# Kernel optimization log

Hardware: AMD Instinct MI355X
Metric: run time of the kernel (lower is better)

Reference implementation:

```python
import jax, jax.numpy as jnp
import numpy as np

N_NODES = 100000
N_EDGES = 3200000
NFEAT, NHID, NCLASS = 512, 256, 40


def setup_inputs() -> dict:
    key = jax.random.key(0)
    ks = jax.random.split(key, 8)
    x = jax.random.normal(ks[0], (N_NODES, NFEAT), dtype=jnp.float32)
    edge_src = jax.random.randint(ks[1], (N_EDGES,), 0, N_NODES, dtype=jnp.int32)
    edge_dst = jax.random.randint(ks[2], (N_EDGES,), 0, N_NODES, dtype=jnp.int32)
    # normalized adjacency values (e.g. D^-1/2 A D^-1/2 entries)
    edge_weight = jax.random.uniform(ks[3], (N_EDGES,), dtype=jnp.float32)
    W1 = jax.random.normal(ks[4], (NFEAT, NHID), dtype=jnp.float32) * (1.0 / np.sqrt(NFEAT))
    b1 = jnp.zeros((NHID,), dtype=jnp.float32)
    W2 = jax.random.normal(ks[5], (NHID, NCLASS), dtype=jnp.float32) * (1.0 / np.sqrt(NHID))
    b2 = jnp.zeros((NCLASS,), dtype=jnp.float32)
    return {"x": x, "edge_src": edge_src, "edge_dst": edge_dst,
            "edge_weight": edge_weight, "W1": W1, "b1": b1, "W2": W2, "b2": b2}


def _gcn_conv(x, edge_src, edge_dst, edge_weight, W, b):
    # GCNConv: support = x @ W ; out = spmm(adj, support) + b
    support = x @ W                                   # [N, D_out]
    msgs = edge_weight[:, None] * support[edge_src]   # [E, D_out]
    agg = jax.ops.segment_sum(msgs, edge_dst, num_segments=x.shape[0])
    return agg + b


def reference(x, edge_src, edge_dst, edge_weight, W1, b1, W2, b2):
    h = jax.nn.relu(_gcn_conv(x, edge_src, edge_dst, edge_weight, W1, b1))
    # F.dropout with training=False is identity (eval/reference mode)
    h = _gcn_conv(h, edge_src, edge_dst, edge_weight, W2, b2)
    return jax.nn.log_softmax(h, axis=1)
```

## Files before the change

kernel.cpp:

```cpp
#include <hip/hip_runtime.h>
#include <hip/hip_bf16.h>
#include <math.h>


#define NFEAT 512
#define NHID  256
#define NCLASS 40
#define BKT_SHIFT 9
#define BKT_NODES 512
#define MAX_BKT 256
#define BIN_EPB 4096

typedef __attribute__((ext_vector_type(4))) float f32x4;
typedef __attribute__((ext_vector_type(8))) short s16x8;

__device__ __forceinline__ ushort f2bf(float f) {
  unsigned u = __float_as_uint(f);
  u = (u + 0x7fffu + ((u >> 16) & 1u)) >> 16;
  return (ushort)u;
}
__device__ __forceinline__ float bflo(unsigned u) {
  return __uint_as_float(u << 16);
}
__device__ __forceinline__ float bfhi(unsigned u) {
  return __uint_as_float(u & 0xffff0000u);
}

__global__ __launch_bounds__(256) void w1t_kernel(const float* __restrict__ W1,
                                                  ushort* __restrict__ Bt) {
  int idx = blockIdx.x * 256 + threadIdx.x;
  int k = idx >> 8, n = idx & 255;
  Bt[n * NFEAT + k] = f2bf(W1[idx]);
}

#define LDK 40
__global__ __launch_bounds__(256) void gemm1_mfma(
    const float* __restrict__ A, const ushort* __restrict__ Bt,
    ushort* __restrict__ C, int M) {
  __shared__ ushort As[128 * LDK];
  __shared__ ushort Bs[128 * LDK];
  int tid = threadIdx.x;
  int wave = tid >> 6, lane = tid & 63;
  int bm = blockIdx.y * 128;
  int bn = blockIdx.x * 128;
  int wm = (wave & 1) * 64, wn = (wave >> 1) * 64;
  int lm = lane & 15;
  int lk = (lane >> 4) * 8;

  int arow = tid >> 1;
  int ahalf = (tid & 1) * 16;
  int brow = tid >> 2;
  int bq = (tid & 3) * 8;

  f32x4 acc[4][4] = {};

  const bool arv = (bm + arow) < M;
  const float* aptr = A + (size_t)(bm + arow) * NFEAT + ahalf;
  ushort* asp = &As[arow * LDK + ahalf];

  for (int k0 = 0; k0 < NFEAT; k0 += 32) {
#pragma unroll
    for (int q = 0; q < 4; ++q) {
      float4 v = arv ? *(const float4*)(aptr + k0 + q * 4)
                     : make_float4(0.f, 0.f, 0.f, 0.f);
      ushort4 b;
      b.x = f2bf(v.x); b.y = f2bf(v.y); b.z = f2bf(v.z); b.w = f2bf(v.w);
      *(ushort4*)(asp + q * 4) = b;
    }
#pragma unroll
    for (int p = 0; p < 2; ++p) {
      int n = p * 64 + brow;
      *(uint4*)&Bs[n * LDK + bq] =
          *(const uint4*)&Bt[(size_t)(bn + n) * NFEAT + k0 + bq];
    }
    __syncthreads();
    s16x8 afr[4], bfr[4];
#pragma unroll
    for (int i = 0; i < 4; ++i)
      afr[i] = *(const s16x8*)&As[(wm + i * 16 + lm) * LDK + lk];
#pragma unroll
    for (int j = 0; j < 4; ++j)
      bfr[j] = *(const s16x8*)&Bs[(wn + j * 16 + lm) * LDK + lk];
#pragma unroll
    for (int i = 0; i < 4; ++i)
#pragma unroll
      for (int j = 0; j < 4; ++j)
        acc[i][j] = __builtin_amdgcn_mfma_f32_16x16x32_bf16(afr[i], bfr[j],
                                                            acc[i][j], 0, 0, 0);
    __syncthreads();
  }
  int ocol = bn + wn + lm;
  int orow0 = bm + wm + (lane >> 4) * 4;
#pragma unroll
  for (int i = 0; i < 4; ++i) {
#pragma unroll
    for (int r = 0; r < 4; ++r) {
      int row = orow0 + i * 16 + r;
      if (row < M) {
#pragma unroll
        for (int j = 0; j < 4; ++j)
          C[(size_t)row * NHID + ocol + j * 16] = f2bf(acc[i][j][r]);
      }
    }
  }
}

__global__ __launch_bounds__(256) void hist_kernel(const int* __restrict__ dst,
                                                   int* __restrict__ deg, int E) {
  int e = blockIdx.x * 256 + threadIdx.x;
  if (e < E) atomicAdd(&deg[dst[e]], 1);
}

__global__ __launch_bounds__(256) void scan1_kernel(const int* __restrict__ deg,
                                                    int* __restrict__ part,
                                                    int* __restrict__ bsums, int M) {
  __shared__ int tmp[256];
  int t = threadIdx.x;
  int i = blockIdx.x * 256 + t;
  int v = (i < M) ? deg[i] : 0;
  tmp[t] = v;
  __syncthreads();
  for (int off = 1; off < 256; off <<= 1) {
    int add = (t >= off) ? tmp[t - off] : 0;
    __syncthreads();
    tmp[t] += add;
    __syncthreads();
  }
  if (i < M) part[i] = tmp[t];
  if (t == 255) bsums[blockIdx.x] = tmp[255];
}

__global__ __launch_bounds__(512) void scan2_kernel(int* __restrict__ bsums, int nb) {
  __shared__ int tmp[512];
  int t = threadIdx.x;
  int v = (t < nb) ? bsums[t] : 0;
  tmp[t] = v;
  __syncthreads();
  for (int off = 1; off < 512; off <<= 1) {
    int add = (t >= off) ? tmp[t - off] : 0;
    __syncthreads();
    tmp[t] += add;
    __syncthreads();
  }
  if (t < nb) bsums[t] = tmp[t];
}

__global__ __launch_bounds__(256) void scan3_kernel(
    const int* __restrict__ part, const int* __restrict__ bsums,
    const int* __restrict__ deg, int* __restrict__ rowptr, int M) {
  int i = blockIdx.x * 256 + threadIdx.x;
  if (i >= M) return;
  int incl = part[i] + (blockIdx.x > 0 ? bsums[blockIdx.x - 1] : 0);
  rowptr[i] = incl - deg[i];
}

__global__ __launch_bounds__(256) void initcur_kernel(
    const int* __restrict__ rowptr, int* __restrict__ gcursor, int nbkt) {
  int b = threadIdx.x;
  if (b < nbkt) gcursor[b] = rowptr[b * BKT_NODES];
}

__global__ __launch_bounds__(256) void binA_kernel(
    const int* __restrict__ esrc, const int* __restrict__ edst,
    const float* __restrict__ ew, int* __restrict__ gcursor,
    int2* __restrict__ tmp_sw, ushort* __restrict__ tmp_d, int E) {
  __shared__ int hist[MAX_BKT];
  int t = threadIdx.x;
  for (int i = t; i < MAX_BKT; i += 256) hist[i] = 0;
  __syncthreads();
  int e0 = blockIdx.x * BIN_EPB;
#pragma unroll
  for (int k = 0; k < BIN_EPB / 256; ++k) {
    int e = e0 + k * 256 + t;
    if (e < E) atomicAdd(&hist[edst[e] >> BKT_SHIFT], 1);
  }
  __syncthreads();
  for (int i = t; i < MAX_BKT; i += 256) {
    int c = hist[i];
    hist[i] = c ? atomicAdd(&gcursor[i], c) : 0;
  }
  __syncthreads();
#pragma unroll
  for (int k = 0; k < BIN_EPB / 256; ++k) {
    int e = e0 + k * 256 + t;
    if (e < E) {
      int d = edst[e];
      int b = d >> BKT_SHIFT;
      int pos = atomicAdd(&hist[b], 1);
      tmp_sw[pos] = make_int2(esrc[e], __float_as_int(ew[e]));
      tmp_d[pos] = (ushort)(d & (BKT_NODES - 1));
    }
  }
}

__global__ __launch_bounds__(512) void binB_kernel(
    const int2* __restrict__ tmp_sw, const ushort* __restrict__ tmp_d,
    const int* __restrict__ rowptr, int2* __restrict__ ep, int M, int E) {
  __shared__ int cur[BKT_NODES];
  int b = blockIdx.x;
  int nbase = b * BKT_NODES;
  for (int i = threadIdx.x; i < BKT_NODES; i += 512) {
    int node = nbase + i;
    cur[i] = (node < M) ? rowptr[node] : 0;
  }
  __syncthreads();
  int start = rowptr[nbase];
  int nend = nbase + BKT_NODES;
  int end = (nend < M) ? rowptr[nend] : E;
  for (int i = start + threadIdx.x; i < end; i += 512) {
    int2 sw = tmp_sw[i];
    int dl = tmp_d[i];
    int pos = atomicAdd(&cur[dl], 1);
    ep[pos] = sw;
  }
}

__global__ __launch_bounds__(256) void spmm1_csr_kernel(
    const ushort* __restrict__ S, const int* __restrict__ rowptr,
    const int* __restrict__ deg, const int2* __restrict__ ep,
    const float* __restrict__ b1, ushort* __restrict__ h, int M) {
  int wid = (blockIdx.x * 256 + threadIdx.x) >> 6;
  int lane = threadIdx.x & 63;
  if (wid >= M) return;
  int beg = rowptr[wid];
  int n = deg[wid];
  const ushort* Sl = S + (size_t)lane * 4;
  float acc0 = 0.f, acc1 = 0.f, acc2 = 0.f, acc3 = 0.f;
  for (int j0 = 0; j0 < n; j0 += 64) {
    int cnt = min(64, n - j0);
    int msrc = 0;
    float mw = 0.f;
    if (lane < cnt) {
      int2 e = ep[beg + j0 + lane];
      msrc = e.x;
      mw = __int_as_float(e.y);
    }
    for (int j = 0; j < cnt; ++j) {
      int s = __shfl(msrc, j);
      float wt = __shfl(mw, j);
      uint2 u = *(const uint2*)(Sl + ((size_t)s << 8));
      acc0 += wt * bflo(u.x);
      acc1 += wt * bfhi(u.x);
      acc2 += wt * bflo(u.y);
      acc3 += wt * bfhi(u.y);
    }
  }
  float4 b = *(const float4*)(b1 + lane * 4);
  ushort4 o;
  o.x = f2bf(fmaxf(acc0 + b.x, 0.f));
  o.y = f2bf(fmaxf(acc1 + b.y, 0.f));
  o.z = f2bf(fmaxf(acc2 + b.z, 0.f));
  o.w = f2bf(fmaxf(acc3 + b.w, 0.f));
  *(ushort4*)(h + ((size_t)wid << 8) + lane * 4) = o;
}

__global__ __launch_bounds__(256) void gemm2_kernel(
    const ushort* __restrict__ H, const float* __restrict__ W2,
    ushort* __restrict__ S2, int M) {
  __shared__ float W2s[NHID * NCLASS];
  for (int i = threadIdx.x; i < NHID * NCLASS; i += 256) W2s[i] = W2[i];
  __syncthreads();
  int row = blockIdx.x * 256 + threadIdx.x;
  if (row >= M) return;
  const float4* W2v = (const float4*)W2s;
  float4 acc[10];
#pragma unroll
  for (int j = 0; j < 10; ++j) acc[j] = make_float4(0.f, 0.f, 0.f, 0.f);
  const uint4* hp = (const uint4*)(H + (size_t)row * NHID);
  for (int kb = 0; kb < 32; ++kb) {
    uint4 u = hp[kb];
    float a[8] = {bflo(u.x), bfhi(u.x), bflo(u.y), bfhi(u.y),
                  bflo(u.z), bfhi(u.z), bflo(u.w), bfhi(u.w)};
#pragma unroll
    for (int kk = 0; kk < 8; ++kk) {
#pragma unroll
      for (int j = 0; j < 10; ++j) {
        float4 wv = W2v[(kb * 8 + kk) * 10 + j];
        acc[j].x += a[kk] * wv.x;
        acc[j].y += a[kk] * wv.y;
        acc[j].z += a[kk] * wv.z;
        acc[j].w += a[kk] * wv.w;
      }
    }
  }
  uint2* outp = (uint2*)(S2 + (size_t)row * NCLASS);
#pragma unroll
  for (int j = 0; j < 10; j += 2) {
    uint2 o0, o1;
    o0.x = (unsigned)f2bf(acc[j].x) | ((unsigned)f2bf(acc[j].y) << 16);
    o0.y = (unsigned)f2bf(acc[j].z) | ((unsigned)f2bf(acc[j].w) << 16);
    o1.x = (unsigned)f2bf(acc[j + 1].x) | ((unsigned)f2bf(acc[j + 1].y) << 16);
    o1.y = (unsigned)f2bf(acc[j + 1].z) | ((unsigned)f2bf(acc[j + 1].w) << 16);
    outp[j] = o0;
    outp[j + 1] = o1;
  }
}

__global__ __launch_bounds__(256) void spmm2_csr_kernel(
    const ushort* __restrict__ S2, const int* __restrict__ rowptr,
    const int* __restrict__ deg, const int2* __restrict__ ep,
    const float* __restrict__ b2, float* __restrict__ out, int M) {
  int wid = (blockIdx.x * 256 + threadIdx.x) >> 6;
  int lane = threadIdx.x & 63;
  if (wid >= M) return;
  int beg = rowptr[wid];
  int n = deg[wid];
  float acc0 = 0.f, acc1 = 0.f;
  const ushort* S2l = S2 + lane * 2;
  for (int j0 = 0; j0 < n; j0 += 64) {
    int cnt = min(64, n - j0);
    int msrc = 0;
    float mw = 0.f;
    if (lane < cnt) {
      int2 e = ep[beg + j0 + lane];
      msrc = e.x;
      mw = __int_as_float(e.y);
    }
    for (int j = 0; j < cnt; ++j) {
      int s = __shfl(msrc, j);
      float wt = __shfl(mw, j);
      if (lane < 20) {
        unsigned u = *(const unsigned*)(S2l + (size_t)s * NCLASS);
        acc0 += wt * bflo(u);
        acc1 += wt * bfhi(u);
      }
    }
  }
  float v0 = -INFINITY, v1 = -INFINITY;
  if (lane < 20) {
    float2 b = *(const float2*)(b2 + lane * 2);
    v0 = acc0 + b.x;
    v1 = acc1 + b.y;
  }
  float m = fmaxf(v0, v1);
#pragma unroll
  for (int off = 32; off; off >>= 1) m = fmaxf(m, __shfl_xor(m, off));
  float ex = (lane < 20) ? __expf(v0 - m) + __expf(v1 - m) : 0.f;
  float s = ex;
#pragma unroll
  for (int off = 32; off; off >>= 1) s += __shfl_xor(s, off);
  float lse = m + __logf(s);
  if (lane < 20) {
    float2 o = {v0 - lse, v1 - lse};
    *(float2*)(out + (size_t)wid * NCLASS + lane * 2) = o;
  }
}

extern "C" void kernel_launch(void* const* d_in, const int* in_sizes, int n_in,
                              void* d_out, int out_size, void* d_ws,
                              size_t ws_size, hipStream_t stream) {
  const float* x  = (const float*)d_in[0];
  const int* esrc = (const int*)d_in[1];
  const int* edst = (const int*)d_in[2];
  const float* ew = (const float*)d_in[3];
  const float* W1 = (const float*)d_in[4];
  const float* b1 = (const float*)d_in[5];
  const float* W2 = (const float*)d_in[6];
  const float* b2 = (const float*)d_in[7];
  float* out = (float*)d_out;

  const int M = in_sizes[0] / NFEAT;
  const int E = in_sizes[1];
  const int nbkt = (M + BKT_NODES - 1) / BKT_NODES;

  char* p = (char*)d_ws;
  ushort* support1 = (ushort*)p;           p += (size_t)M * NHID * 2;
  ushort* h        = (ushort*)p;           p += (size_t)M * NHID * 2;
  ushort* support2 = (ushort*)p;           p += (size_t)M * NCLASS * 2;
  ushort* W1t      = (ushort*)p;           p += (size_t)NFEAT * NHID * 2;
  int*    deg      = (int*)p;              p += (size_t)M * 4;
  int*    part     = (int*)p;              p += (size_t)M * 4;
  int*    rowptr   = (int*)p;              p += (size_t)M * 4;
  int*    gcursor  = (int*)p;              p += MAX_BKT * 4;
  int*    bsums    = (int*)p;              p += 512 * 4;
  int2*   ep       = (int2*)p;             p += (size_t)E * 8;
  int2*   tmp_sw   = (int2*)p;             p += (size_t)E * 8;
  ushort* tmp_d    = (ushort*)p;

  const int nbScan = (M + 255) / 256;

  hipMemsetAsync(deg, 0, (size_t)M * sizeof(int), stream);
  hist_kernel<<<(E + 255) / 256, 256, 0, stream>>>(edst, deg, E);
  scan1_kernel<<<nbScan, 256, 0, stream>>>(deg, part, bsums, M);
  scan2_kernel<<<1, 512, 0, stream>>>(bsums, nbScan);
  scan3_kernel<<<nbScan, 256, 0, stream>>>(part, bsums, deg, rowptr, M);
  initcur_kernel<<<1, 256, 0, stream>>>(rowptr, gcursor, nbkt);
  binA_kernel<<<(E + BIN_EPB - 1) / BIN_EPB, 256, 0, stream>>>(
      esrc, edst, ew, gcursor, tmp_sw, tmp_d, E);
  binB_kernel<<<nbkt, 512, 0, stream>>>(tmp_sw, tmp_d, rowptr, ep, M, E);

  w1t_kernel<<<(NFEAT * NHID) / 256, 256, 0, stream>>>(W1, W1t);
  dim3 g1(NHID / 128, (M + 127) / 128);
  gemm1_mfma<<<g1, 256, 0, stream>>>(x, W1t, support1, M);
  spmm1_csr_kernel<<<(M * 64 + 255) / 256, 256, 0, stream>>>(
      support1, rowptr, deg, ep, b1, h, M);

  gemm2_kernel<<<(M + 255) / 256, 256, 0, stream>>>(h, W2, support2, M);
  spmm2_csr_kernel<<<(M * 64 + 255) / 256, 256, 0, stream>>>(
      support2, rowptr, deg, ep, b2, out, M);
}
```

Measured before the change: 1.125 ms.

## Split SpMM waves across edges with wider gathers and unrolled loads

In the first-layer SpMM, each half of the 64-lane wave now takes a different edge. Each lane gathers 8 bf16 features with a 16-byte load, four edges are loaded per iteration, and the two halves are combined with a cross-half shuffle at the end. In the second-layer SpMM, three groups of 20 lanes each process a different edge, so 60 of 64 lanes are busy instead of 20, and partial sums are reduced by shuffles before the log-softmax. The aim is more memory-level parallelism and better lane use in these gather-bound kernels. The cost is extra shuffles and reductions. Inactive lanes 60–63 compute addresses slightly past the row, which may read just beyond the end of the last row.

```diff
diff --git a/kernel.cpp b/kernel.cpp
--- a/kernel.cpp
+++ b/kernel.cpp
@@ -215,6 +215,12 @@
   }
 }
 
+#define ACC8(UV, WT)                                            \
+  acc[0] += (WT) * bflo((UV).x); acc[1] += (WT) * bfhi((UV).x); \
+  acc[2] += (WT) * bflo((UV).y); acc[3] += (WT) * bfhi((UV).y); \
+  acc[4] += (WT) * bflo((UV).z); acc[5] += (WT) * bfhi((UV).z); \
+  acc[6] += (WT) * bflo((UV).w); acc[7] += (WT) * bfhi((UV).w);
+
 __global__ __launch_bounds__(256) void spmm1_csr_kernel(
     const ushort* __restrict__ S, const int* __restrict__ rowptr,
     const int* __restrict__ deg, const int2* __restrict__ ep,
@@ -224,8 +230,10 @@
   if (wid >= M) return;
   int beg = rowptr[wid];
   int n = deg[wid];
-  const ushort* Sl = S + (size_t)lane * 4;
-  float acc0 = 0.f, acc1 = 0.f, acc2 = 0.f, acc3 = 0.f;
+  int half = lane >> 5;
+  int fl = lane & 31;
+  const ushort* Sl = S + (size_t)fl * 8;
+  float acc[8] = {};
   for (int j0 = 0; j0 < n; j0 += 64) {
     int cnt = min(64, n - j0);
     int msrc = 0;
@@ -235,23 +243,37 @@
       msrc = e.x;
       mw = __int_as_float(e.y);
     }
-    for (int j = 0; j < cnt; ++j) {
-      int s = __shfl(msrc, j);
-      float wt = __shfl(mw, j);
-      uint2 u = *(const uint2*)(Sl + ((size_t)s << 8));
-      acc0 += wt * bflo(u.x);
-      acc1 += wt * bfhi(u.x);
-      acc2 += wt * bflo(u.y);
-      acc3 += wt * bfhi(u.y);
-    }
-  }
-  float4 b = *(const float4*)(b1 + lane * 4);
+    int pairs = (cnt + 1) >> 1;
+    for (int p = 0; p < pairs; p += 4) {
+      int jj0 = 2 * p + half;
+      int s0 = __shfl(msrc, jj0);     float w0 = __shfl(mw, jj0);
+      int s1 = __shfl(msrc, jj0 + 2); float w1 = __shfl(mw, jj0 + 2);
+      int s2 = __shfl(msrc, jj0 + 4); float w2 = __shfl(mw, jj0 + 4);
+      int s3 = __shfl(msrc, jj0 + 6); float w3 = __shfl(mw, jj0 + 6);
+      uint4 u0 = *(const uint4*)(Sl + ((size_t)s0 << 8));
+      uint4 u1 = *(const uint4*)(Sl + ((size_t)s1 << 8));
+      uint4 u2 = *(const uint4*)(Sl + ((size_t)s2 << 8));
+      uint4 u3 = *(const uint4*)(Sl + ((size_t)s3 << 8));
+      ACC8(u0, w0)
+      ACC8(u1, w1)
+      ACC8(u2, w2)
+      ACC8(u3, w3)
+    }
+  }
+#pragma unroll
+  for (int k = 0; k < 8; ++k) acc[k] += __shfl_xor(acc[k], 32);
+  float a0 = half ? acc[4] : acc[0];
+  float a1 = half ? acc[5] : acc[1];
+  float a2 = half ? acc[6] : acc[2];
+  float a3 = half ? acc[7] : acc[3];
+  int fb = fl * 8 + half * 4;
+  float4 b = *(const float4*)(b1 + fb);
   ushort4 o;
-  o.x = f2bf(fmaxf(acc0 + b.x, 0.f));
-  o.y = f2bf(fmaxf(acc1 + b.y, 0.f));
-  o.z = f2bf(fmaxf(acc2 + b.z, 0.f));
-  o.w = f2bf(fmaxf(acc3 + b.w, 0.f));
-  *(ushort4*)(h + ((size_t)wid << 8) + lane * 4) = o;
+  o.x = f2bf(fmaxf(a0 + b.x, 0.f));
+  o.y = f2bf(fmaxf(a1 + b.y, 0.f));
+  o.z = f2bf(fmaxf(a2 + b.z, 0.f));
+  o.w = f2bf(fmaxf(a3 + b.w, 0.f));
+  *(ushort4*)(h + ((size_t)wid << 8) + fb) = o;
 }
 
 __global__ __launch_bounds__(256) void gemm2_kernel(
@@ -305,8 +327,11 @@
   if (wid >= M) return;
   int beg = rowptr[wid];
   int n = deg[wid];
+  int g = (lane >= 40) ? 2 : ((lane >= 20) ? 1 : 0);
+  bool act = lane < 60;
+  int cl = lane - 20 * g;
+  const ushort* S2l = S2 + cl * 2;
   float acc0 = 0.f, acc1 = 0.f;
-  const ushort* S2l = S2 + lane * 2;
   for (int j0 = 0; j0 < n; j0 += 64) {
     int cnt = min(64, n - j0);
     int msrc = 0;
@@ -316,21 +341,29 @@
       msrc = e.x;
       mw = __int_as_float(e.y);
     }
-    for (int j = 0; j < cnt; ++j) {
-      int s = __shfl(msrc, j);
-      float wt = __shfl(mw, j);
-      if (lane < 20) {
-        unsigned u = *(const unsigned*)(S2l + (size_t)s * NCLASS);
-        acc0 += wt * bflo(u);
-        acc1 += wt * bfhi(u);
-      }
-    }
-  }
+    int trips = (cnt + 2) / 3;
+    for (int p = 0; p < trips; p += 2) {
+      int ja = 3 * p + g;
+      int jb = ja + 3;
+      int sa = __shfl(msrc, ja & 63); float wa = __shfl(mw, ja & 63);
+      int sb = __shfl(msrc, jb & 63); float wb = __shfl(mw, jb & 63);
+      wa = (act && ja < cnt) ? wa : 0.f;
+      wb = (act && jb < cnt) ? wb : 0.f;
+      unsigned ua = *(const unsigned*)(S2l + (size_t)sa * NCLASS);
+      unsigned ub = *(const unsigned*)(S2l + (size_t)sb * NCLASS);
+      acc0 += wa * bflo(ua) + wb * bflo(ub);
+      acc1 += wa * bfhi(ua) + wb * bfhi(ub);
+    }
+  }
+  float r0a = __shfl(acc0, (lane + 20) & 63);
+  float r0b = __shfl(acc0, (lane + 40) & 63);
+  float r1a = __shfl(acc1, (lane + 20) & 63);
+  float r1b = __shfl(acc1, (lane + 40) & 63);
   float v0 = -INFINITY, v1 = -INFINITY;
   if (lane < 20) {
     float2 b = *(const float2*)(b2 + lane * 2);
-    v0 = acc0 + b.x;
-    v1 = acc1 + b.y;
+    v0 = acc0 + r0a + r0b + b.x;
+    v1 = acc1 + r1a + r1b + b.y;
   }
   float m = fmaxf(v0, v1);
 #pragma unroll
```

After: 988.4 us. -12.1%, faster.
